# Performance work log

Measured on AMD Instinct MI355X. Metric: run time of the kernel, lower is better.

The kernel has to match this reference:

```python
import jax, jax.numpy as jnp
import numpy as np

C = 256
B = 8
N = 2048
EPS_BN = 1e-5


def _bn(x, g, b):
    # BatchNorm1d in training mode: stats over (batch, length) per channel
    m = x.mean(axis=(0, 2), keepdims=True)
    v = ((x - m) ** 2).mean(axis=(0, 2), keepdims=True)
    return g[None, :, None] * (x - m) / jnp.sqrt(v + EPS_BN) + b[None, :, None]


def _sa_layer(x, wqk, wv, bv, wt, bt, g, b):
    # shared q/k projection (q_conv.weight = k_conv.weight in the original)
    q = jnp.einsum('oc,bcn->bon', wqk, x)          # [B, C//4, N]
    energy = jnp.einsum('bcm,bcn->bmn', q, q)      # x_q^T x_k -> [B, N, N]
    att = jax.nn.softmax(energy, axis=-1)
    att = att / (1e-9 + att.sum(axis=1, keepdims=True))  # L1 renorm over dim=1
    v = jnp.einsum('oc,bcn->bon', wv, x) + bv[None, :, None]
    x_r = jnp.einsum('bcm,bmn->bcn', v, att)       # [B, C, N]
    t = jnp.einsum('oc,bcn->bon', wt, x - x_r) + bt[None, :, None]
    x_r = jax.nn.relu(_bn(t, g, b))
    return x + x_r


def setup_inputs() -> dict:
    key = jax.random.key(0)
    ks = jax.random.split(key, 16)
    s = lambda k, shp, scale: jax.random.normal(k, shp, dtype=jnp.float32) * scale
    inp = {
        'x': s(ks[0], (B, C, N), 1.0),
        'conv1_w': s(ks[1], (C, C), 1.0 / np.sqrt(C)),
        'conv2_w': s(ks[2], (C, C), 1.0 / np.sqrt(C)),
        'bn1_g': jnp.ones((C,), jnp.float32),
        'bn1_b': jnp.zeros((C,), jnp.float32),
        'bn2_g': jnp.ones((C,), jnp.float32),
        'bn2_b': jnp.zeros((C,), jnp.float32),
        'sa_wqk': s(ks[3], (4, C // 4, C), 1.0 / np.sqrt(C)),
        'sa_wv': s(ks[4], (4, C, C), 1.0 / np.sqrt(C)),
        'sa_bv': s(ks[5], (4, C), 0.01),
        'sa_wt': s(ks[6], (4, C, C), 1.0 / np.sqrt(C)),
        'sa_bt': s(ks[7], (4, C), 0.01),
        'sa_g': jnp.ones((4, C), jnp.float32),
        'sa_b': jnp.zeros((4, C), jnp.float32),
    }
    return inp


def reference(x, conv1_w, conv2_w, bn1_g, bn1_b, bn2_g, bn2_b,
              sa_wqk, sa_wv, sa_bv, sa_wt, sa_bt, sa_g, sa_b):
    x = jax.nn.relu(_bn(jnp.einsum('oc,bcn->bon', conv1_w, x), bn1_g, bn1_b))
    x = jax.nn.relu(_bn(jnp.einsum('oc,bcn->bon', conv2_w, x), bn2_g, bn2_b))
    outs = []
    for i in range(4):  # four structurally identical SA layers, small fixed loop
        x = _sa_layer(x, sa_wqk[i], sa_wv[i], sa_bv[i], sa_wt[i], sa_bt[i],
                      sa_g[i], sa_b[i])
        outs.append(x)
    return jnp.concatenate(outs, axis=1)  # [B, 4*C, N]
```

## Files before the change

### kernel.cpp

```cpp
#include <hip/hip_runtime.h>
#include <hip/hip_bf16.h>

typedef __attribute__((ext_vector_type(8))) short short8;
typedef __attribute__((ext_vector_type(4))) float f32x4;
using bf16 = __hip_bfloat16;

constexpr int C  = 256;
constexpr int BB = 8;
constexpr int NN = 2048;

#define DEVI __device__ __forceinline__

DEVI short8 ldg8(const bf16* p) { return *reinterpret_cast<const short8*>(p); }

DEVI f32x4 mfma16(short8 a, short8 b, f32x4 c) {
  return __builtin_amdgcn_mfma_f32_16x16x32_bf16(a, b, c, 0, 0, 0);
}

DEVI void split2(float x, bf16& h, bf16& l) {
  h = __float2bfloat16(x);
  l = __float2bfloat16(x - __bfloat162float(h));
}

DEVI short b2s(bf16 x) { short s; __builtin_memcpy(&s, &x, 2); return s; }


DEVI void store_tile16(const float v[4], bf16* __restrict__ H, bf16* __restrict__ L,
                       size_t tilebase, float* lds, int lane) {
  int l15 = lane & 15, l4 = lane >> 4;
#pragma unroll
  for (int r = 0; r < 4; ++r) lds[(l4 * 4 + r) * 20 + l15] = v[r];
  asm volatile("s_waitcnt lgkmcnt(0)" ::: "memory");
  __builtin_amdgcn_sched_barrier(0);
  int n = lane & 15, cg = (lane >> 4) & 1, pl = lane >> 5;
  short8 o;
#pragma unroll
  for (int j = 0; j < 8; ++j) {
    bf16 h, l;
    split2(lds[n * 20 + cg * 8 + j], h, l);
    o[j] = pl ? b2s(l) : b2s(h);
  }
  bf16* P = pl ? L : H;
  *reinterpret_cast<short8*>(P + tilebase + (size_t)cg * 128 + n * 8) = o;
}

__global__ __launch_bounds__(256) void k_cvtW(const float* __restrict__ s,
                                              bf16* __restrict__ dh,
                                              bf16* __restrict__ dl, int rows) {
  int idx = blockIdx.x * 256 + threadIdx.x;
  if (idx >= rows * 32) return;
  int row = idx >> 5, kg = idx & 31;
  const float* sp = s + row * 256 + kg * 8;
  short8 oh, ol;
#pragma unroll
  for (int j = 0; j < 8; ++j) {
    bf16 h, l;
    split2(sp[j], h, l);
    oh[j] = b2s(h); ol[j] = b2s(l);
  }
  size_t off = ((size_t)(row >> 4) * 32 + kg) * 128 + (row & 15) * 8;
  *reinterpret_cast<short8*>(dh + off) = oh;
  *reinterpret_cast<short8*>(dl + off) = ol;
}

__global__ __launch_bounds__(256) void k_tin(const float* __restrict__ x,
                                             bf16* __restrict__ Xh,
                                             bf16* __restrict__ Xl) {
  __shared__ float tile[64][65];
  int b = blockIdx.z, n0 = blockIdx.x * 64, c0 = blockIdx.y * 64;
  int t = threadIdx.x;
  int tn = t & 63, tq = t >> 6;
#pragma unroll
  for (int i = 0; i < 16; ++i) {
    int cc = i * 4 + tq;
    tile[cc][tn] = x[((size_t)(b * C + c0 + cc)) * NN + n0 + tn];
  }
  __syncthreads();
  bf16* XHb = Xh + (size_t)b * NN * C;
  bf16* XLb = Xl + (size_t)b * NN * C;
#pragma unroll
  for (int i = 0; i < 4; ++i) {
    int e = i * 256 + t;
    int nl = e & 63;
    int cgp = e >> 6;
    int cg = cgp & 7, pl = cgp >> 3;
    short8 o;
#pragma unroll
    for (int j = 0; j < 8; ++j) {
      bf16 h, l;
      split2(tile[cg * 8 + j][nl], h, l);
      o[j] = pl ? b2s(l) : b2s(h);
    }
    int n = n0 + nl;
    size_t off = ((size_t)(n >> 4) * 32 + ((c0 >> 3) + cg)) * 128 + (n & 15) * 8;
    bf16* P = pl ? XLb : XHb;
    *reinterpret_cast<short8*>(P + off) = o;
  }
}

template <bool BIASJ, bool STATS>
__global__ __launch_bounds__(512, 4) void k_gemm_tr(const bf16* __restrict__ Ah,
                                                    const bf16* __restrict__ Al,
                                                    const bf16* __restrict__ Wh,
                                                    const bf16* __restrict__ Wl,
                                                    const float* __restrict__ bias,
                                                    float* __restrict__ OutF, int OD,
                                                    float* __restrict__ sS,
                                                    float* __restrict__ sS2) {
  __shared__ short8 smW[4096];
  __shared__ float smS[64], smS2[64];
  int b = blockIdx.x, i0 = blockIdx.y * 128, j0 = blockIdx.z * 64;
  int t = threadIdx.x, lane = t & 63, w = t >> 6;
  int l15 = lane & 15, l4 = lane >> 4;
  if (STATS && t < 64) { smS[t] = 0.f; smS2[t] = 0.f; }
  size_t wbase = (size_t)(j0 >> 4) * 4096;
  for (int i = t; i < 2048; i += 512) {
    smW[i]        = ldg8(Wh + wbase + (size_t)i * 8);
    smW[2048 + i] = ldg8(Wl + wbase + (size_t)i * 8);
  }
  __syncthreads();
  const bf16* Abh = Ah + (size_t)b * NN * C;
  const bf16* Abl = Al + (size_t)b * NN * C;
  int ntile = (i0 >> 4) + w;
  f32x4 acc[4];
#pragma unroll
  for (int ct = 0; ct < 4; ++ct) acc[ct] = f32x4{0.f, 0.f, 0.f, 0.f};
#pragma unroll
  for (int ks = 0; ks < 8; ++ks) {
    int ko = ks * 4 + l4;
    short8 a_h = ldg8(Abh + ((size_t)ntile * 32 + ko) * 128 + l15 * 8);
    short8 a_l = ldg8(Abl + ((size_t)ntile * 32 + ko) * 128 + l15 * 8);
#pragma unroll
    for (int ct = 0; ct < 4; ++ct) {
      short8 w_h = smW[ct * 512 + ko * 16 + l15];
      short8 w_l = smW[2048 + ct * 512 + ko * 16 + l15];
      acc[ct] = mfma16(a_h, w_h, acc[ct]);
      acc[ct] = mfma16(a_h, w_l, acc[ct]);
      acc[ct] = mfma16(a_l, w_h, acc[ct]);
    }
  }
#pragma unroll
  for (int ct = 0; ct < 4; ++ct) {
    float bj = 0.f;
    if (BIASJ) bj = bias[j0 + ct * 16 + l15];
    float s = 0.f, s2 = 0.f;
#pragma unroll
    for (int r = 0; r < 4; ++r) {
      float v = acc[ct][r] + bj;
      int row = i0 + w * 16 + l4 * 4 + r;
      OutF[((size_t)(b * NN + row)) * OD + j0 + ct * 16 + l15] = v;
      if (STATS) { s += v; s2 += v * v; }
    }
    if (STATS) {
      s += __shfl_xor(s, 16); s2 += __shfl_xor(s2, 16);
      s += __shfl_xor(s, 32); s2 += __shfl_xor(s2, 32);
      if (l4 == 0) {
        atomicAdd(&smS[ct * 16 + l15], s);
        atomicAdd(&smS2[ct * 16 + l15], s2);
      }
    }
  }
  if (STATS) {
    __syncthreads();
    if (t < 64) {
      atomicAdd(&sS[j0 + t], smS[t]);
      atomicAdd(&sS2[j0 + t], smS2[t]);
    }
  }
}

__global__ __launch_bounds__(256) void k_qproj(const bf16* __restrict__ Xh,
                                               const bf16* __restrict__ Xl,
                                               const bf16* __restrict__ Wh,
                                               const bf16* __restrict__ Wl,
                                               bf16* __restrict__ Qh,
                                               bf16* __restrict__ Ql) {
  __shared__ float scratch[4][320];
  int b = blockIdx.x, ntile = blockIdx.y;
  int t = threadIdx.x, lane = t & 63, w = t >> 6;
  int l15 = lane & 15, l4 = lane >> 4;
  const bf16* Abh = Xh + (size_t)b * NN * C;
  const bf16* Abl = Xl + (size_t)b * NN * C;
  f32x4 acc = {0.f, 0.f, 0.f, 0.f};
#pragma unroll
  for (int ks = 0; ks < 8; ++ks) {
    int ko = ks * 4 + l4;
    short8 a_h = ldg8(Abh + ((size_t)ntile * 32 + ko) * 128 + l15 * 8);
    short8 a_l = ldg8(Abl + ((size_t)ntile * 32 + ko) * 128 + l15 * 8);
    size_t wo = ((size_t)w * 32 + ko) * 128 + l15 * 8;
    short8 w_h = ldg8(Wh + wo);
    short8 w_l = ldg8(Wl + wo);
    acc = mfma16(a_h, w_h, acc);
    acc = mfma16(a_h, w_l, acc);
    acc = mfma16(a_l, w_h, acc);
  }
  float v[4] = {acc[0], acc[1], acc[2], acc[3]};
  size_t tb = ((size_t)ntile * 8 + w * 2) * 128;
  store_tile16(v, Qh + (size_t)b * NN * 64, Ql + (size_t)b * NN * 64, tb,
               scratch[w], lane);
}

__global__ __launch_bounds__(512, 4) void k_gemm_nm(const bf16* __restrict__ Wh,
                                                    const bf16* __restrict__ Wl,
                                                    const bf16* __restrict__ Xh,
                                                    const bf16* __restrict__ Xl,
                                                    const float* __restrict__ bias,
                                                    bf16* __restrict__ Vh,
                                                    bf16* __restrict__ Vl) {
  __shared__ short8 smX[4096];
  __shared__ float scratch[8][320];
  int b = blockIdx.x, i0 = blockIdx.y * 128, j0 = blockIdx.z * 64;
  int t = threadIdx.x, lane = t & 63, w = t >> 6;
  int l15 = lane & 15, l4 = lane >> 4;
  const bf16* Xbh = Xh + (size_t)b * NN * C;
  const bf16* Xbl = Xl + (size_t)b * NN * C;
  size_t xbase = (size_t)(j0 >> 4) * 4096;
  for (int i = t; i < 2048; i += 512) {
    smX[i]        = ldg8(Xbh + xbase + (size_t)i * 8);
    smX[2048 + i] = ldg8(Xbl + xbase + (size_t)i * 8);
  }
  __syncthreads();
  int ntile = (i0 >> 4) + w;
  f32x4 acc[4];
#pragma unroll
  for (int ct = 0; ct < 4; ++ct) acc[ct] = f32x4{0.f, 0.f, 0.f, 0.f};
#pragma unroll
  for (int ks = 0; ks < 8; ++ks) {
    int ko = ks * 4 + l4;
    short8 a_h = ldg8(Wh + ((size_t)ntile * 32 + ko) * 128 + l15 * 8);
    short8 a_l = ldg8(Wl + ((size_t)ntile * 32 + ko) * 128 + l15 * 8);
#pragma unroll
    for (int ct = 0; ct < 4; ++ct) {
      short8 x_h = smX[ct * 512 + ko * 16 + l15];
      short8 x_l = smX[2048 + ct * 512 + ko * 16 + l15];
      acc[ct] = mfma16(a_h, x_h, acc[ct]);
      acc[ct] = mfma16(a_h, x_l, acc[ct]);
      acc[ct] = mfma16(a_l, x_h, acc[ct]);
    }
  }
  float br[4];
#pragma unroll
  for (int r = 0; r < 4; ++r) br[r] = bias[i0 + w * 16 + l4 * 4 + r];
  bf16* Vbh = Vh + (size_t)b * C * NN;
  bf16* Vbl = Vl + (size_t)b * C * NN;
#pragma unroll
  for (int ct = 0; ct < 4; ++ct) {
    float v[4];
#pragma unroll
    for (int r = 0; r < 4; ++r) v[r] = acc[ct][r] + br[r];
    size_t tb = ((size_t)ntile * (NN >> 3) + ((j0 + ct * 16) >> 3)) * 128;
    store_tile16(v, Vbh, Vbl, tb, scratch[w], lane);
  }
}

__global__ __launch_bounds__(256) void k_rowstats(const bf16* __restrict__ Qh,
                                                  const bf16* __restrict__ Ql,
                                                  float* __restrict__ rm,
                                                  float* __restrict__ irs) {
  __shared__ float redM[4][16], redS[4][16];
  int b = blockIdx.x;
  int t = threadIdx.x, lane = t & 63, w = t >> 6;
  int l15 = lane & 15, l4 = lane >> 4;
  int mt = blockIdx.y;
  const bf16* QHb = Qh + (size_t)b * NN * 64;
  const bf16* QLb = Ql + (size_t)b * NN * 64;
  short8 ah0 = ldg8(QHb + ((size_t)mt * 8 + l4) * 128 + l15 * 8);
  short8 ah1 = ldg8(QHb + ((size_t)mt * 8 + 4 + l4) * 128 + l15 * 8);
  short8 al0 = ldg8(QLb + ((size_t)mt * 8 + l4) * 128 + l15 * 8);
  short8 al1 = ldg8(QLb + ((size_t)mt * 8 + 4 + l4) * 128 + l15 * 8);
  float lmax[4], lsum[4];
#pragma unroll
  for (int r = 0; r < 4; ++r) { lmax[r] = -3.4e38f; lsum[r] = 0.f; }
  for (int nb = w * 32; nb < w * 32 + 32; ++nb) {
    short8 bh0 = ldg8(QHb + ((size_t)nb * 8 + l4) * 128 + l15 * 8);
    short8 bh1 = ldg8(QHb + ((size_t)nb * 8 + 4 + l4) * 128 + l15 * 8);
    short8 bl0 = ldg8(QLb + ((size_t)nb * 8 + l4) * 128 + l15 * 8);
    short8 bl1 = ldg8(QLb + ((size_t)nb * 8 + 4 + l4) * 128 + l15 * 8);
    f32x4 e = {0.f, 0.f, 0.f, 0.f};
    e = mfma16(ah0, bh0, e); e = mfma16(ah1, bh1, e);
    e = mfma16(ah0, bl0, e); e = mfma16(ah1, bl1, e);
    e = mfma16(al0, bh0, e); e = mfma16(al1, bh1, e);
#pragma unroll
    for (int r = 0; r < 4; ++r) {
      float v = e[r];
      float nm = fmaxf(lmax[r], v);
      lsum[r] = lsum[r] * __expf(lmax[r] - nm) + __expf(v - nm);
      lmax[r] = nm;
    }
  }
#pragma unroll
  for (int r = 0; r < 4; ++r) {
    for (int mk = 1; mk < 16; mk <<= 1) {
      float om = __shfl_xor(lmax[r], mk, 16);
      float os = __shfl_xor(lsum[r], mk, 16);
      float nm = fmaxf(lmax[r], om);
      lsum[r] = lsum[r] * __expf(lmax[r] - nm) + os * __expf(om - nm);
      lmax[r] = nm;
    }
  }
  if (l15 == 0) {
#pragma unroll
    for (int r = 0; r < 4; ++r) {
      redM[w][l4 * 4 + r] = lmax[r];
      redS[w][l4 * 4 + r] = lsum[r];
    }
  }
  __syncthreads();
  if (t < 16) {
    float m = redM[0][t];
    m = fmaxf(m, redM[1][t]); m = fmaxf(m, redM[2][t]); m = fmaxf(m, redM[3][t]);
    float s = 0.f;
#pragma unroll
    for (int w2 = 0; w2 < 4; ++w2) s += redS[w2][t] * __expf(redM[w2][t] - m);
    rm[b * NN + mt * 16 + t] = m;
    irs[b * NN + mt * 16 + t] = 1.0f / s;
  }
}

__global__ __launch_bounds__(512, 4) void k_attnY(const bf16* __restrict__ QH,
                                                  const bf16* __restrict__ QL,
                                                  const bf16* __restrict__ VH,
                                                  const bf16* __restrict__ VL,
                                                  const float* __restrict__ rm,
                                                  const float* __restrict__ irs,
                                                  const float* __restrict__ Xf,
                                                  bf16* __restrict__ DH,
                                                  bf16* __restrict__ DL) {
  __shared__ bf16 Pb[2][32 * 136];
  __shared__ float rmL[2048], irL[2048];
  __shared__ float colLds[32];
  __shared__ float scratch[8][320];
  int bid = blockIdx.x;
  int b = bid & 7, n0 = (bid >> 3) * 32;
  int t = threadIdx.x, lane = t & 63, w = t >> 6;
  int l15 = lane & 15, l4 = lane >> 4;
  int nt = w >> 2, pp = w & 3;
  const bf16* QHb = QH + (size_t)b * NN * 64;
  const bf16* QLb = QL + (size_t)b * NN * 64;
  const bf16* VHb = VH + (size_t)b * C * NN;
  const bf16* VLb = VL + (size_t)b * C * NN;
  for (int i = t; i < NN; i += 512) {
    rmL[i] = rm[b * NN + i];
    irL[i] = irs[b * NN + i];
  }
  if (t < 32) colLds[t] = 0.f;
  int ntq = (n0 >> 4) + nt;
  short8 qh0 = ldg8(QHb + ((size_t)ntq * 8 + l4) * 128 + l15 * 8);
  short8 qh1 = ldg8(QHb + ((size_t)ntq * 8 + 4 + l4) * 128 + l15 * 8);
  short8 ql0 = ldg8(QLb + ((size_t)ntq * 8 + l4) * 128 + l15 * 8);
  short8 ql1 = ldg8(QLb + ((size_t)ntq * 8 + 4 + l4) * 128 + l15 * 8);
  f32x4 zero = {0.f, 0.f, 0.f, 0.f};
  f32x4 acc[2][2];
#pragma unroll
  for (int a = 0; a < 2; ++a)
#pragma unroll
    for (int ct = 0; ct < 2; ++ct) acc[a][ct] = zero;
  float cac[4] = {0.f, 0.f, 0.f, 0.f};
  __syncthreads();
  for (int s = 0; s < 16; ++s) {
    bf16* pbw = Pb[s & 1];
#pragma unroll
    for (int sub = 0; sub < 2; ++sub) {
      int mt8 = pp * 2 + sub;
      int gmt = s * 8 + mt8;
      short8 bh0 = ldg8(QHb + ((size_t)gmt * 8 + l4) * 128 + l15 * 8);
      short8 bh1 = ldg8(QHb + ((size_t)gmt * 8 + 4 + l4) * 128 + l15 * 8);
      short8 bl0 = ldg8(QLb + ((size_t)gmt * 8 + l4) * 128 + l15 * 8);
      short8 bl1 = ldg8(QLb + ((size_t)gmt * 8 + 4 + l4) * 128 + l15 * 8);
      f32x4 eA = zero, eB = zero;
      eA = mfma16(qh0, bh0, eA); eB = mfma16(qh1, bh1, eB);
      eA = mfma16(qh0, bl0, eA); eB = mfma16(qh1, bl1, eB);
      eA = mfma16(ql0, bh0, eA); eB = mfma16(ql1, bh1, eB);
      float rmv = rmL[gmt * 16 + l15], iv = irL[gmt * 16 + l15];
      int blk = nt * 16 + mt8 * 2 + (l15 >> 3);
#pragma unroll
      for (int r = 0; r < 4; ++r) {
        float p = __expf(eA[r] + eB[r] - rmv) * iv;
        bf16 ph = __float2bfloat16(p);
        cac[r] += __bfloat162float(ph);
        pbw[blk * 136 + (l4 * 4 + r) * 8 + (l15 & 7)] = ph;
      }
    }
    short8 vhA[2][2], vlA[2][2];
#pragma unroll
    for (int kc = 0; kc < 2; ++kc)
#pragma unroll
      for (int ct = 0; ct < 2; ++ct) {
        size_t vo = ((size_t)(w * 2 + ct) * 256 + s * 16 + kc * 4 + l4) * 128 + l15 * 8;
        vhA[kc][ct] = ldg8(VHb + vo);
        vlA[kc][ct] = ldg8(VLb + vo);
      }
    asm volatile("s_waitcnt lgkmcnt(0)" ::: "memory");
    __builtin_amdgcn_sched_barrier(0);
    __builtin_amdgcn_s_barrier();
    short8 vhB[2][2], vlB[2][2];
#pragma unroll
    for (int kc = 0; kc < 2; ++kc)
#pragma unroll
      for (int ct = 0; ct < 2; ++ct) {
        size_t vo = ((size_t)(w * 2 + ct) * 256 + s * 16 + (kc + 2) * 4 + l4) * 128 + l15 * 8;
        vhB[kc][ct] = ldg8(VHb + vo);
        vlB[kc][ct] = ldg8(VLb + vo);
      }
#pragma unroll
    for (int kc = 0; kc < 2; ++kc) {
      short8 pa0 = *reinterpret_cast<const short8*>(&pbw[(kc * 4 + l4) * 136 + l15 * 8]);
      short8 pa1 = *reinterpret_cast<const short8*>(&pbw[(16 + kc * 4 + l4) * 136 + l15 * 8]);
#pragma unroll
      for (int ct = 0; ct < 2; ++ct) {
        acc[0][ct] = mfma16(pa0, vhA[kc][ct], acc[0][ct]);
        acc[0][ct] = mfma16(pa0, vlA[kc][ct], acc[0][ct]);
        acc[1][ct] = mfma16(pa1, vhA[kc][ct], acc[1][ct]);
        acc[1][ct] = mfma16(pa1, vlA[kc][ct], acc[1][ct]);
      }
    }
#pragma unroll
    for (int kc = 0; kc < 2; ++kc) {
      short8 pa0 = *reinterpret_cast<const short8*>(&pbw[((kc + 2) * 4 + l4) * 136 + l15 * 8]);
      short8 pa1 = *reinterpret_cast<const short8*>(&pbw[(16 + (kc + 2) * 4 + l4) * 136 + l15 * 8]);
#pragma unroll
      for (int ct = 0; ct < 2; ++ct) {
        acc[0][ct] = mfma16(pa0, vhB[kc][ct], acc[0][ct]);
        acc[0][ct] = mfma16(pa0, vlB[kc][ct], acc[0][ct]);
        acc[1][ct] = mfma16(pa1, vhB[kc][ct], acc[1][ct]);
        acc[1][ct] = mfma16(pa1, vlB[kc][ct], acc[1][ct]);
      }
    }
  }
#pragma unroll
  for (int r = 0; r < 4; ++r) {
    float v2 = cac[r];
    v2 += __shfl_xor(v2, 1, 16); v2 += __shfl_xor(v2, 2, 16);
    v2 += __shfl_xor(v2, 4, 16); v2 += __shfl_xor(v2, 8, 16);
    if (l15 == 0) atomicAdd(&colLds[nt * 16 + l4 * 4 + r], v2);
  }
  __syncthreads();
  if (t < 32) colLds[t] = 1.0f / (1e-9f + colLds[t]);
  __syncthreads();
  bf16* DHb = DH + (size_t)b * NN * C;
  bf16* DLb = DL + (size_t)b * NN * C;
#pragma unroll
  for (int a = 0; a < 2; ++a) {
#pragma unroll
    for (int ct = 0; ct < 2; ++ct) {
      float d[4];
      int cidx = w * 32 + ct * 16 + l15;
#pragma unroll
      for (int r = 0; r < 4; ++r) {
        int n = n0 + a * 16 + l4 * 4 + r;
        d[r] = Xf[((size_t)(b * NN + n)) * C + cidx] -
               acc[a][ct][r] * colLds[a * 16 + l4 * 4 + r];
      }
      size_t tb = ((size_t)((n0 >> 4) + a) * 32 + ((w * 32 + ct * 16) >> 3)) * 128;
      store_tile16(d, DHb, DLb, tb, scratch[w], lane);
    }
  }
}

template <bool RES>
__global__ __launch_bounds__(256) void k_bnrelu(const float* __restrict__ Tt,
                                                const float* __restrict__ sS,
                                                const float* __restrict__ sS2,
                                                const float* __restrict__ g,
                                                const float* __restrict__ bb,
                                                float* __restrict__ Xf,
                                                bf16* __restrict__ Xh,
                                                bf16* __restrict__ Xl,
                                                float* __restrict__ outp, int Loff) {
  __shared__ float vb[16][257];
  int b = blockIdx.x, n0 = blockIdx.y * 16;
  int c = threadIdx.x;
  float cnt = (float)(BB * NN);
  float mean = sS[c] / cnt;
  float var = fmaxf(sS2[c] / cnt - mean * mean, 0.f);
  float sc = g[c] * rsqrtf(var + 1e-5f);
  float sh = bb[c] - mean * sc;
#pragma unroll
  for (int i = 0; i < 16; ++i) {
    int n = n0 + i;
    size_t idx = ((size_t)(b * NN + n)) * C + c;
    float v = Tt[idx] * sc + sh;
    v = fmaxf(v, 0.f);
    if (RES) v += Xf[idx];
    Xf[idx] = v;
    bf16 h, l;
    split2(v, h, l);
    size_t off = (size_t)b * NN * C +
                 ((size_t)(n >> 4) * 32 + (c >> 3)) * 128 + (n & 15) * 8 + (c & 7);
    Xh[off] = h;
    Xl[off] = l;
    if (RES) vb[i][c] = v;
  }
  if (RES) {
    __syncthreads();
    int nl = threadIdx.x & 15, cb = threadIdx.x >> 4;
#pragma unroll
    for (int j = 0; j < 16; ++j) {
      int cc = cb + j * 16;
      outp[((size_t)(b * 1024 + Loff + cc)) * NN + n0 + nl] = vb[nl][cc];
    }
  }
}

extern "C" void kernel_launch(void* const* d_in, const int* in_sizes, int n_in,
                              void* d_out, int out_size, void* d_ws, size_t ws_size,
                              hipStream_t stream) {
  const float* x       = (const float*)d_in[0];
  const float* conv1_w = (const float*)d_in[1];
  const float* conv2_w = (const float*)d_in[2];
  const float* bn1_g   = (const float*)d_in[3];
  const float* bn1_b   = (const float*)d_in[4];
  const float* bn2_g   = (const float*)d_in[5];
  const float* bn2_b   = (const float*)d_in[6];
  const float* wqk     = (const float*)d_in[7];
  const float* wv      = (const float*)d_in[8];
  const float* bv      = (const float*)d_in[9];
  const float* wt      = (const float*)d_in[10];
  const float* bt      = (const float*)d_in[11];
  const float* sg      = (const float*)d_in[12];
  const float* sb      = (const float*)d_in[13];
  float* out = (float*)d_out;

  char* p = (char*)d_ws;
  auto take = [&](size_t n) { char* r = p; p += n; return r; };
  bf16* WB1h = (bf16*)take(131072);
  bf16* WB1l = (bf16*)take(131072);
  bf16* WB2h = (bf16*)take(131072);
  bf16* WB2l = (bf16*)take(131072);
  bf16* WBQh = (bf16*)take(131072);
  bf16* WBQl = (bf16*)take(131072);
  bf16* WBVh = (bf16*)take(524288);
  bf16* WBVl = (bf16*)take(524288);
  bf16* WBTh = (bf16*)take(524288);
  bf16* WBTl = (bf16*)take(524288);
  bf16* XTh  = (bf16*)take(8388608);
  bf16* XTl  = (bf16*)take(8388608);
  float* XF  = (float*)take(16777216);
  bf16* QTh  = (bf16*)take(2097152);
  bf16* QTl  = (bf16*)take(2097152);
  bf16* VBh  = (bf16*)take(8388608);
  bf16* VBl  = (bf16*)take(8388608);
  float* TT  = (float*)VBh;
  bf16* DTh  = (bf16*)take(8388608);
  bf16* DTl  = (bf16*)take(8388608);
  float* RM   = (float*)take(65536);
  float* IRS  = (float*)take(65536);
  float* STAT = (float*)take(12288);

  hipMemsetAsync(STAT, 0, 6 * 512 * sizeof(float), stream);
  k_cvtW<<<32, 256, 0, stream>>>(conv1_w, WB1h, WB1l, 256);
  k_cvtW<<<32, 256, 0, stream>>>(conv2_w, WB2h, WB2l, 256);
  k_cvtW<<<32, 256, 0, stream>>>(wqk, WBQh, WBQl, 256);
  k_cvtW<<<128, 256, 0, stream>>>(wv, WBVh, WBVl, 1024);
  k_cvtW<<<128, 256, 0, stream>>>(wt, WBTh, WBTl, 1024);
  k_tin<<<dim3(32, 4, 8), 256, 0, stream>>>(x, XTh, XTl);

  k_gemm_tr<false, true><<<dim3(8, 16, 4), 512, 0, stream>>>(
      XTh, XTl, WB1h, WB1l, nullptr, TT, 256, STAT + 0, STAT + 256);
  k_bnrelu<false><<<dim3(8, 128), 256, 0, stream>>>(TT, STAT + 0, STAT + 256, bn1_g, bn1_b,
                                                    XF, XTh, XTl, nullptr, 0);

  k_gemm_tr<false, true><<<dim3(8, 16, 4), 512, 0, stream>>>(
      XTh, XTl, WB2h, WB2l, nullptr, TT, 256, STAT + 512, STAT + 768);
  k_bnrelu<false><<<dim3(8, 128), 256, 0, stream>>>(TT, STAT + 512, STAT + 768, bn2_g, bn2_b,
                                                    XF, XTh, XTl, nullptr, 0);

  for (int L = 0; L < 4; ++L) {
    float* ST = STAT + (2 + L) * 512;
    k_qproj<<<dim3(8, 128), 256, 0, stream>>>(XTh, XTl, WBQh + L * 16384,
                                              WBQl + L * 16384, QTh, QTl);
    k_gemm_nm<<<dim3(8, 2, 32), 512, 0, stream>>>(WBVh + L * 65536, WBVl + L * 65536,
                                                  XTh, XTl, bv + L * 256, VBh, VBl);
    k_rowstats<<<dim3(8, 128), 256, 0, stream>>>(QTh, QTl, RM, IRS);
    k_attnY<<<512, 512, 0, stream>>>(QTh, QTl, VBh, VBl, RM, IRS, XF, DTh, DTl);
    k_gemm_tr<true, true><<<dim3(8, 16, 4), 512, 0, stream>>>(
        DTh, DTl, WBTh + L * 65536, WBTl + L * 65536, bt + L * 256, TT, 256, ST, ST + 256);
    k_bnrelu<true><<<dim3(8, 128), 256, 0, stream>>>(TT, ST, ST + 256, sg + L * 256,
                                                     sb + L * 256, XF, XTh, XTl, out,
                                                     L * 256);
  }
}
```

Before: 626.0 us.

## Drop fp32 activation copy, prefetch attention Q tiles, merge weight conversion launches

Removes the separate fp32 activation buffer. The residual and x-x_r terms are rebuilt from the existing bf16 hi/lo split pair, which cuts an extra 16MB read and write per stage. In k_attnY the Q fragments for the next step are loaded one iteration ahead, after the barrier, so their latency overlaps the V MFMA work. The five weight-conversion launches are merged into one kernel. Rebuilding activations from hi+lo is slightly less exact than fp32, and the extra prefetch registers may pressure occupancy.

Measured after the change: 748.1 us. 19.5% more time.

```diff
diff --git a/kernel.cpp b/kernel.cpp
--- a/kernel.cpp
+++ b/kernel.cpp
@@ -44,11 +44,20 @@
   *reinterpret_cast<short8*>(P + tilebase + (size_t)cg * 128 + n * 8) = o;
 }
 
-__global__ __launch_bounds__(256) void k_cvtW(const float* __restrict__ s,
-                                              bf16* __restrict__ dh,
-                                              bf16* __restrict__ dl, int rows) {
+__global__ __launch_bounds__(256) void k_cvtW5(
+    const float* __restrict__ s0, const float* __restrict__ s1,
+    const float* __restrict__ s2, const float* __restrict__ s3,
+    const float* __restrict__ s4, bf16* __restrict__ h0, bf16* __restrict__ l0,
+    bf16* __restrict__ h1, bf16* __restrict__ l1, bf16* __restrict__ h2,
+    bf16* __restrict__ l2, bf16* __restrict__ h3, bf16* __restrict__ l3,
+    bf16* __restrict__ h4, bf16* __restrict__ l4) {
   int idx = blockIdx.x * 256 + threadIdx.x;
-  if (idx >= rows * 32) return;
+  const float* s; bf16 *dh, *dl;
+  if (idx < 8192)        { s = s0; dh = h0; dl = l0; }
+  else if (idx < 16384)  { s = s1; dh = h1; dl = l1; idx -= 8192; }
+  else if (idx < 24576)  { s = s2; dh = h2; dl = l2; idx -= 16384; }
+  else if (idx < 57344)  { s = s3; dh = h3; dl = l3; idx -= 24576; }
+  else                   { s = s4; dh = h4; dl = l4; idx -= 57344; }
   int row = idx >> 5, kg = idx & 31;
   const float* sp = s + row * 256 + kg * 8;
   short8 oh, ol;
@@ -323,7 +332,8 @@
                                                   const bf16* __restrict__ VL,
                                                   const float* __restrict__ rm,
                                                   const float* __restrict__ irs,
-                                                  const float* __restrict__ Xf,
+                                                  const bf16* __restrict__ XH,
+                                                  const bf16* __restrict__ XL,
                                                   bf16* __restrict__ DH,
                                                   bf16* __restrict__ DL) {
   __shared__ bf16 Pb[2][32 * 136];
@@ -356,23 +366,29 @@
 #pragma unroll
     for (int ct = 0; ct < 2; ++ct) acc[a][ct] = zero;
   float cac[4] = {0.f, 0.f, 0.f, 0.f};
+
+#define LDE(D, GMT)                                                       \
+  D[0] = ldg8(QHb + ((size_t)(GMT) * 8 + l4) * 128 + l15 * 8);            \
+  D[1] = ldg8(QHb + ((size_t)(GMT) * 8 + 4 + l4) * 128 + l15 * 8);        \
+  D[2] = ldg8(QLb + ((size_t)(GMT) * 8 + l4) * 128 + l15 * 8);            \
+  D[3] = ldg8(QLb + ((size_t)(GMT) * 8 + 4 + l4) * 128 + l15 * 8);
+
+  short8 ef0[4], ef1[4];
+  LDE(ef0, pp * 2)
+  LDE(ef1, pp * 2 + 1)
   __syncthreads();
   for (int s = 0; s < 16; ++s) {
     bf16* pbw = Pb[s & 1];
 #pragma unroll
     for (int sub = 0; sub < 2; ++sub) {
-      int mt8 = pp * 2 + sub;
-      int gmt = s * 8 + mt8;
-      short8 bh0 = ldg8(QHb + ((size_t)gmt * 8 + l4) * 128 + l15 * 8);
-      short8 bh1 = ldg8(QHb + ((size_t)gmt * 8 + 4 + l4) * 128 + l15 * 8);
-      short8 bl0 = ldg8(QLb + ((size_t)gmt * 8 + l4) * 128 + l15 * 8);
-      short8 bl1 = ldg8(QLb + ((size_t)gmt * 8 + 4 + l4) * 128 + l15 * 8);
+      const short8* F = sub ? ef1 : ef0;
+      int gmt = s * 8 + pp * 2 + sub;
       f32x4 eA = zero, eB = zero;
-      eA = mfma16(qh0, bh0, eA); eB = mfma16(qh1, bh1, eB);
-      eA = mfma16(qh0, bl0, eA); eB = mfma16(qh1, bl1, eB);
-      eA = mfma16(ql0, bh0, eA); eB = mfma16(ql1, bh1, eB);
+      eA = mfma16(qh0, F[0], eA); eB = mfma16(qh1, F[1], eB);
+      eA = mfma16(qh0, F[2], eA); eB = mfma16(qh1, F[3], eB);
+      eA = mfma16(ql0, F[0], eA); eB = mfma16(ql1, F[1], eB);
       float rmv = rmL[gmt * 16 + l15], iv = irL[gmt * 16 + l15];
-      int blk = nt * 16 + mt8 * 2 + (l15 >> 3);
+      int blk = nt * 16 + (pp * 2 + sub) * 2 + (l15 >> 3);
 #pragma unroll
       for (int r = 0; r < 4; ++r) {
         float p = __expf(eA[r] + eB[r] - rmv) * iv;
@@ -393,6 +409,10 @@
     asm volatile("s_waitcnt lgkmcnt(0)" ::: "memory");
     __builtin_amdgcn_sched_barrier(0);
     __builtin_amdgcn_s_barrier();
+    if (s < 15) {
+      LDE(ef0, (s + 1) * 8 + pp * 2)
+      LDE(ef1, (s + 1) * 8 + pp * 2 + 1)
+    }
     short8 vhB[2][2], vlB[2][2];
 #pragma unroll
     for (int kc = 0; kc < 2; ++kc)
@@ -427,6 +447,7 @@
       }
     }
   }
+#undef LDE
 #pragma unroll
   for (int r = 0; r < 4; ++r) {
     float v2 = cac[r];
@@ -437,6 +458,8 @@
   __syncthreads();
   if (t < 32) colLds[t] = 1.0f / (1e-9f + colLds[t]);
   __syncthreads();
+  const bf16* XHb = XH + (size_t)b * NN * C;
+  const bf16* XLb = XL + (size_t)b * NN * C;
   bf16* DHb = DH + (size_t)b * NN * C;
   bf16* DLb = DL + (size_t)b * NN * C;
 #pragma unroll
@@ -448,8 +471,9 @@
 #pragma unroll
       for (int r = 0; r < 4; ++r) {
         int n = n0 + a * 16 + l4 * 4 + r;
-        d[r] = Xf[((size_t)(b * NN + n)) * C + cidx] -
-               acc[a][ct][r] * colLds[a * 16 + l4 * 4 + r];
+        size_t off = ((size_t)(n >> 4) * 32 + (cidx >> 3)) * 128 + (n & 15) * 8 + (cidx & 7);
+        float xv = __bfloat162float(XHb[off]) + __bfloat162float(XLb[off]);
+        d[r] = xv - acc[a][ct][r] * colLds[a * 16 + l4 * 4 + r];
       }
       size_t tb = ((size_t)((n0 >> 4) + a) * 32 + ((w * 32 + ct * 16) >> 3)) * 128;
       store_tile16(d, DHb, DLb, tb, scratch[w], lane);
@@ -463,7 +487,6 @@
                                                 const float* __restrict__ sS2,
                                                 const float* __restrict__ g,
                                                 const float* __restrict__ bb,
-                                                float* __restrict__ Xf,
                                                 bf16* __restrict__ Xh,
                                                 bf16* __restrict__ Xl,
                                                 float* __restrict__ outp, int Loff) {
@@ -481,12 +504,11 @@
     size_t idx = ((size_t)(b * NN + n)) * C + c;
     float v = Tt[idx] * sc + sh;
     v = fmaxf(v, 0.f);
-    if (RES) v += Xf[idx];
-    Xf[idx] = v;
+    size_t off = (size_t)b * NN * C +
+                 ((size_t)(n >> 4) * 32 + (c >> 3)) * 128 + (n & 15) * 8 + (c & 7);
+    if (RES) v += __bfloat162float(Xh[off]) + __bfloat162float(Xl[off]);
     bf16 h, l;
     split2(v, h, l);
-    size_t off = (size_t)b * NN * C +
-                 ((size_t)(n >> 4) * 32 + (c >> 3)) * 128 + (n & 15) * 8 + (c & 7);
     Xh[off] = h;
     Xl[off] = l;
     if (RES) vb[i][c] = v;
@@ -535,7 +557,6 @@
   bf16* WBTl = (bf16*)take(524288);
   bf16* XTh  = (bf16*)take(8388608);
   bf16* XTl  = (bf16*)take(8388608);
-  float* XF  = (float*)take(16777216);
   bf16* QTh  = (bf16*)take(2097152);
   bf16* QTl  = (bf16*)take(2097152);
   bf16* VBh  = (bf16*)take(8388608);
@@ -548,22 +569,20 @@
   float* STAT = (float*)take(12288);
 
   hipMemsetAsync(STAT, 0, 6 * 512 * sizeof(float), stream);
-  k_cvtW<<<32, 256, 0, stream>>>(conv1_w, WB1h, WB1l, 256);
-  k_cvtW<<<32, 256, 0, stream>>>(conv2_w, WB2h, WB2l, 256);
-  k_cvtW<<<32, 256, 0, stream>>>(wqk, WBQh, WBQl, 256);
-  k_cvtW<<<128, 256, 0, stream>>>(wv, WBVh, WBVl, 1024);
-  k_cvtW<<<128, 256, 0, stream>>>(wt, WBTh, WBTl, 1024);
+  k_cvtW5<<<352, 256, 0, stream>>>(conv1_w, conv2_w, wqk, wv, wt,
+                                   WB1h, WB1l, WB2h, WB2l, WBQh, WBQl,
+                                   WBVh, WBVl, WBTh, WBTl);
   k_tin<<<dim3(32, 4, 8), 256, 0, stream>>>(x, XTh, XTl);
 
   k_gemm_tr<false, true><<<dim3(8, 16, 4), 512, 0, stream>>>(
       XTh, XTl, WB1h, WB1l, nullptr, TT, 256, STAT + 0, STAT + 256);
   k_bnrelu<false><<<dim3(8, 128), 256, 0, stream>>>(TT, STAT + 0, STAT + 256, bn1_g, bn1_b,
-                                                    XF, XTh, XTl, nullptr, 0);
+                                                    XTh, XTl, nullptr, 0);
 
   k_gemm_tr<false, true><<<dim3(8, 16, 4), 512, 0, stream>>>(
       XTh, XTl, WB2h, WB2l, nullptr, TT, 256, STAT + 512, STAT + 768);
   k_bnrelu<false><<<dim3(8, 128), 256, 0, stream>>>(TT, STAT + 512, STAT + 768, bn2_g, bn2_b,
-                                                    XF, XTh, XTl, nullptr, 0);
+                                                    XTh, XTl, nullptr, 0);
 
   for (int L = 0; L < 4; ++L) {
     float* ST = STAT + (2 + L) * 512;
@@ -572,11 +591,11 @@
     k_gemm_nm<<<dim3(8, 2, 32), 512, 0, stream>>>(WBVh + L * 65536, WBVl + L * 65536,
                                                   XTh, XTl, bv + L * 256, VBh, VBl);
     k_rowstats<<<dim3(8, 128), 256, 0, stream>>>(QTh, QTl, RM, IRS);
-    k_attnY<<<512, 512, 0, stream>>>(QTh, QTl, VBh, VBl, RM, IRS, XF, DTh, DTl);
+    k_attnY<<<512, 512, 0, stream>>>(QTh, QTl, VBh, VBl, RM, IRS, XTh, XTl, DTh, DTl);
     k_gemm_tr<true, true><<<dim3(8, 16, 4), 512, 0, stream>>>(
         DTh, DTl, WBTh + L * 65536, WBTl + L * 65536, bt + L * 256, TT, 256, ST, ST + 256);
     k_bnrelu<true><<<dim3(8, 128), 256, 0, stream>>>(TT, ST, ST + 256, sg + L * 256,
-                                                     sb + L * 256, XF, XTh, XTl, out,
+                                                     sb + L * 256, XTh, XTl, out,
                                                      L * 256);
   }
 }
```
